# Kernel tuning notes

Measured on AMD Instinct MI355X. Metric: run time of the kernel, lower is better.

Reference implementation:

```python
import jax, jax.numpy as jnp
import numpy as np

BATCH, SEQ_LEN, INPUT_DIM = 64, 8192, 1
RESERVOIR_DIM = 80
DELAY_TAPS = [1, 4, 24, 96, 168]
MAX_DELAY = max(DELAY_TAPS)
SPECTRAL_RADIUS = 0.9
INPUT_SCALING = 0.5
LEAK_RATE = 0.3
SEED = 42
# buf[:, MAX_DELAY - tau] holds h_{t - tau} (zeros if t - tau < 0)
TAP_IDX = np.array([MAX_DELAY - tau for tau in DELAY_TAPS])


def setup_inputs() -> dict:
    key = jax.random.key(0)
    x = jax.random.normal(key, (BATCH, SEQ_LEN, INPUT_DIM), dtype=jnp.float32)
    rng = np.random.default_rng(SEED)
    W_in = rng.uniform(-INPUT_SCALING, INPUT_SCALING, size=(RESERVOIR_DIM, INPUT_DIM))
    W_fb_list = []
    for tau in DELAY_TAPS:
        W_k = rng.standard_normal((RESERVOIR_DIM, RESERVOIR_DIM))
        max_eig = np.max(np.abs(np.linalg.eigvals(W_k)))
        if max_eig > 0:
            W_k = W_k * (SPECTRAL_RADIUS / len(DELAY_TAPS)) / max_eig
        W_fb_list.append(W_k)
    W_fb = np.stack(W_fb_list, axis=0)  # (K, R, R)
    bias = rng.uniform(-0.1, 0.1, size=RESERVOIR_DIM)
    return {
        "x": x,
        "W_in": jnp.asarray(W_in, dtype=jnp.float32),
        "W_fb": jnp.asarray(W_fb, dtype=jnp.float32),
        "bias": jnp.asarray(bias, dtype=jnp.float32),
    }


def reference(x, W_in, W_fb, bias):
    B, S, _ = x.shape
    R = W_in.shape[0]
    # Precompute input drive for all timesteps: (S, B, R) for scan over time.
    drive = jnp.einsum("bsi,ri->sbr", x, W_in)
    h0 = jnp.zeros((B, R), dtype=x.dtype)
    buf0 = jnp.zeros((B, MAX_DELAY, R), dtype=x.dtype)  # rolling history

    def step(carry, drive_t):
        h, buf = carry
        delayed = buf[:, TAP_IDX, :]  # (B, K, R): h_{t-tau} for each tap
        # feedback = sum_k delayed_k @ W_fb_k.T
        feedback = jnp.einsum("bkj,kij->bi", delayed, W_fb)
        h_new = (1.0 - LEAK_RATE) * h + LEAK_RATE * jnp.tanh(drive_t + feedback + bias)
        buf = jnp.concatenate([buf[:, 1:], h_new[:, None, :]], axis=1)
        return (h_new, buf), h_new

    (_, _), states = jax.lax.scan(step, (h0, buf0), drive)
    return jnp.transpose(states, (1, 0, 2))  # (B, S, R)
```

## Files before the change

kernel.cpp:

```cpp
#include <hip/hip_runtime.h>

#define BATCH 64
#define SEQ 8192
#define RDIM 80
#define RING 169
#define NCHUNK (SEQ / 2)

typedef float v2f __attribute__((ext_vector_type(2)));

__device__ __forceinline__ float fast_tanh(float z) {
    float e = __expf(2.0f * z);
    return 1.0f - 2.0f / (e + 1.0f);
}

template <int CTRL>
__device__ __forceinline__ float dpp_xor_add(float v) {
    int o = __builtin_amdgcn_mov_dpp(__float_as_int(v), CTRL, 0xF, 0xF, true);
    return v + __int_as_float(o);
}

__global__ __launch_bounds__(256, 1)
void reservoir_kernel(const float* __restrict__ x,
                      const float* __restrict__ W_in,
                      const float* __restrict__ W_fb,
                      const float* __restrict__ bias,
                      float* __restrict__ out) {
    __shared__ __align__(16) float ring[RING * RDIM];
    __shared__ __align__(16) float h_hist[4 * RDIM];

    const int b    = blockIdx.x;
    const int t    = threadIdx.x;
    const int wid  = t >> 6;
    const int lane = t & 63;

    for (int i = t; i < RING * RDIM; i += 256) ring[i] = 0.0f;
    for (int i = t; i < 4 * RDIM; i += 256) h_hist[i] = 0.0f;

    const float* xb   = x + (size_t)b * SEQ;
    float*       outb = out + (size_t)b * (size_t)SEQ * RDIM;

    v2f wr2[80];

    int q = 0, sub = 0, rowA = 0, rowB = 0;
    float hA = 0.f, hB = 0.f, winA = 0.f, winB = 0.f, bA = 0.f, bB = 0.f;
    v2f hh2[10];
    int tap_tau = 0, qq = 0, half = 0;
    bool tap_valid = false, tap_lo = false;
    float x0 = 0.f, x1 = 0.f;

    if (wid == 0) {
        q = lane >> 2; sub = lane & 3;
        rowA = 5 * q + sub;
        rowB = 5 * q + 4;
        #pragma unroll
        for (int r = 0; r < 5; ++r) {
            const float* src = W_fb + (size_t)(5 * q + r) * RDIM + 20 * sub;
            #pragma unroll
            for (int j4 = 0; j4 < 5; ++j4) {
                float4 v = ((const float4*)src)[j4];
                wr2[r * 10 + 2 * j4 + 0] = (v2f){v.x, v.y};
                wr2[r * 10 + 2 * j4 + 1] = (v2f){v.z, v.w};
            }
        }
        winA = W_in[rowA]; bA = bias[rowA];
        winB = W_in[rowB]; bB = bias[rowB];
        #pragma unroll
        for (int j2 = 0; j2 < 10; ++j2) hh2[j2] = (v2f){0.f, 0.f};
        x0 = xb[0]; x1 = xb[1];
    } else {
        int g = (wid - 1) * 64 + lane;
        tap_valid = (g < 160);
        int gg = tap_valid ? g : 159;
        int k = gg / 40, rem = gg % 40;
        qq = rem >> 1; half = rem & 1;
        tap_lo = (half == 0);
        const int taus[4] = {4, 24, 96, 168};
        tap_tau = taus[k];
        #pragma unroll
        for (int r = 0; r < 4; ++r) {
            const float* src = W_fb + (size_t)(k + 1) * RDIM * RDIM
                                    + (size_t)(4 * qq + r) * RDIM + 40 * half;
            #pragma unroll
            for (int j4 = 0; j4 < 10; ++j4) {
                float4 v = ((const float4*)src)[j4];
                wr2[r * 20 + 2 * j4 + 0] = (v2f){v.x, v.y};
                wr2[r * 20 + 2 * j4 + 1] = (v2f){v.z, v.w};
            }
        }
    }

    __syncthreads();

    for (int c = 0; c < NCHUNK; ++c) {
        if (wid == 0) {
            const int s0  = 2 * c;
            const int sl0 = s0 % RING, sl1 = (s0 + 1) % RING;
            float rgA0 = ring[sl0 * RDIM + rowA];
            float rgA1 = ring[sl1 * RDIM + rowA];
            float rgB0 = 0.f, rgB1 = 0.f;
            if (sub == 0) { rgB0 = ring[sl0 * RDIM + rowB]; rgB1 = ring[sl1 * RDIM + rowB]; }
            ring[sl0 * RDIM + rowA] = 0.f; ring[sl1 * RDIM + rowA] = 0.f;
            if (sub == 0) { ring[sl0 * RDIM + rowB] = 0.f; ring[sl1 * RDIM + rowB] = 0.f; }
            float xn0 = x0, xn1 = x1;
            if (s0 + 2 < SEQ) { float2 xn = *(const float2*)(xb + s0 + 2); xn0 = xn.x; xn1 = xn.y; }

            #pragma unroll
            for (int st = 0; st < 2; ++st) {
                const int s     = s0 + st;
                const float xs  = st ? x1   : x0;
                const float rgA = st ? rgA1 : rgA0;
                const float rgB = st ? rgB1 : rgB0;
                v2f dd2[5];
                #pragma unroll
                for (int r = 0; r < 5; ++r) dd2[r] = (v2f){0.f, 0.f};
                #pragma unroll
                for (int r = 0; r < 5; ++r)
                    #pragma unroll
                    for (int j2 = 0; j2 < 10; ++j2)
                        dd2[r] = __builtin_elementwise_fma(wr2[r * 10 + j2], hh2[j2], dd2[r]);
                float dd[5];
                #pragma unroll
                for (int r = 0; r < 5; ++r) dd[r] = dd2[r].x + dd2[r].y;
                #pragma unroll
                for (int r = 0; r < 5; ++r) {
                    dd[r] = dpp_xor_add<0xB1>(dd[r]);
                    dd[r] = dpp_xor_add<0x4E>(dd[r]);
                }
                float dA = (sub == 0) ? dd[0] : (sub == 1) ? dd[1] : (sub == 2) ? dd[2] : dd[3];
                float zA = dA + rgA + bA + xs * winA;
                hA = 0.7f * hA + 0.3f * fast_tanh(zA);
                if (sub == 0) {
                    float zB = dd[4] + rgB + bB + xs * winB;
                    hB = 0.7f * hB + 0.3f * fast_tanh(zB);
                }
                h_hist[(s & 3) * RDIM + rowA] = hA;
                if (sub == 0) h_hist[(s & 3) * RDIM + rowB] = hB;
                {
                    const float4* hp = (const float4*)(h_hist + (s & 3) * RDIM + 20 * sub);
                    #pragma unroll
                    for (int j4 = 0; j4 < 5; ++j4) {
                        float4 v = hp[j4];
                        hh2[2 * j4 + 0] = (v2f){v.x, v.y};
                        hh2[2 * j4 + 1] = (v2f){v.z, v.w};
                    }
                }
                outb[(size_t)s * RDIM + rowA] = hA;
                if (sub == 0) outb[(size_t)s * RDIM + rowB] = hB;
            }
            x0 = xn0; x1 = xn1;
        } else if (c > 0) {
            const int sp0 = 2 * (c - 1);
            #pragma unroll
            for (int st = 0; st < 2; ++st) {
                const int sp = sp0 + st;
                const float* hp = h_hist + (sp & 3) * RDIM + 40 * half;
                v2f ha2[20];
                #pragma unroll
                for (int j4 = 0; j4 < 10; ++j4) {
                    float4 v = ((const float4*)hp)[j4];
                    ha2[2 * j4 + 0] = (v2f){v.x, v.y};
                    ha2[2 * j4 + 1] = (v2f){v.z, v.w};
                }
                v2f dA2[4];
                #pragma unroll
                for (int r = 0; r < 4; ++r) dA2[r] = (v2f){0.f, 0.f};
                #pragma unroll
                for (int r = 0; r < 4; ++r)
                    #pragma unroll
                    for (int j2 = 0; j2 < 20; ++j2)
                        dA2[r] = __builtin_elementwise_fma(wr2[r * 20 + j2], ha2[j2], dA2[r]);
                float dA[4];
                #pragma unroll
                for (int r = 0; r < 4; ++r) dA[r] = dA2[r].x + dA2[r].y;
                #pragma unroll
                for (int r = 0; r < 4; ++r)
                    dA[r] = dpp_xor_add<0xB1>(dA[r]);
                if (tap_valid && tap_lo) {
                    const int sl = (sp + tap_tau) % RING;
                    float4* pA = (float4*)(ring + sl * RDIM + 4 * qq);
                    float4 vA = *pA;
                    vA.x += dA[0]; vA.y += dA[1]; vA.z += dA[2]; vA.w += dA[3];
                    *pA = vA;
                }
            }
        }
        asm volatile("s_waitcnt lgkmcnt(0)" ::: "memory");
        __builtin_amdgcn_s_barrier();
    }
}

extern "C" void kernel_launch(void* const* d_in, const int* in_sizes, int n_in,
                              void* d_out, int out_size, void* d_ws, size_t ws_size,
                              hipStream_t stream) {
    const float* x    = (const float*)d_in[0];
    const float* W_in = (const float*)d_in[1];
    const float* W_fb = (const float*)d_in[2];
    const float* bias = (const float*)d_in[3];
    float* out        = (float*)d_out;

    reservoir_kernel<<<BATCH, 256, 0, stream>>>(x, W_in, W_fb, bias, out);
}
```

Measured before the change: 3.452 ms.

## Pack two batch elements per 512-thread workgroup

Each workgroup now processes two batch rows with separate ring and history buffers in shared memory, launching half as many blocks with twice the threads. The intent is to share the per-step barrier and improve CU/SIMD utilization. It risks coupling the two recurrences on one barrier and reducing available registers per thread.

```diff
diff --git a/kernel.cpp b/kernel.cpp
--- a/kernel.cpp
+++ b/kernel.cpp
@@ -19,22 +19,27 @@
     return v + __int_as_float(o);
 }
 
-__global__ __launch_bounds__(256, 1)
+__global__ __attribute__((amdgpu_flat_work_group_size(512, 512)))
 void reservoir_kernel(const float* __restrict__ x,
                       const float* __restrict__ W_in,
                       const float* __restrict__ W_fb,
                       const float* __restrict__ bias,
                       float* __restrict__ out) {
-    __shared__ __align__(16) float ring[RING * RDIM];
-    __shared__ __align__(16) float h_hist[4 * RDIM];
-
-    const int b    = blockIdx.x;
+    __shared__ __align__(16) float ring[2 * RING * RDIM];
+    __shared__ __align__(16) float h_hist[2 * 4 * RDIM];
+
     const int t    = threadIdx.x;
     const int wid  = t >> 6;
     const int lane = t & 63;
-
-    for (int i = t; i < RING * RDIM; i += 256) ring[i] = 0.0f;
-    for (int i = t; i < 4 * RDIM; i += 256) h_hist[i] = 0.0f;
+    const int bh   = wid >> 2;
+    const int role = wid & 3;
+    const int b    = blockIdx.x * 2 + bh;
+
+    for (int i = t; i < 2 * RING * RDIM; i += 512) ring[i] = 0.0f;
+    for (int i = t; i < 2 * 4 * RDIM; i += 512) h_hist[i] = 0.0f;
+
+    float* ringp = ring + bh * (RING * RDIM);
+    float* hhp   = h_hist + bh * (4 * RDIM);
 
     const float* xb   = x + (size_t)b * SEQ;
     float*       outb = out + (size_t)b * (size_t)SEQ * RDIM;
@@ -48,7 +53,7 @@
     bool tap_valid = false, tap_lo = false;
     float x0 = 0.f, x1 = 0.f;
 
-    if (wid == 0) {
+    if (role == 0) {
         q = lane >> 2; sub = lane & 3;
         rowA = 5 * q + sub;
         rowB = 5 * q + 4;
@@ -68,7 +73,7 @@
         for (int j2 = 0; j2 < 10; ++j2) hh2[j2] = (v2f){0.f, 0.f};
         x0 = xb[0]; x1 = xb[1];
     } else {
-        int g = (wid - 1) * 64 + lane;
+        int g = (role - 1) * 64 + lane;
         tap_valid = (g < 160);
         int gg = tap_valid ? g : 159;
         int k = gg / 40, rem = gg % 40;
@@ -92,15 +97,15 @@
     __syncthreads();
 
     for (int c = 0; c < NCHUNK; ++c) {
-        if (wid == 0) {
+        if (role == 0) {
             const int s0  = 2 * c;
             const int sl0 = s0 % RING, sl1 = (s0 + 1) % RING;
-            float rgA0 = ring[sl0 * RDIM + rowA];
-            float rgA1 = ring[sl1 * RDIM + rowA];
+            float rgA0 = ringp[sl0 * RDIM + rowA];
+            float rgA1 = ringp[sl1 * RDIM + rowA];
             float rgB0 = 0.f, rgB1 = 0.f;
-            if (sub == 0) { rgB0 = ring[sl0 * RDIM + rowB]; rgB1 = ring[sl1 * RDIM + rowB]; }
-            ring[sl0 * RDIM + rowA] = 0.f; ring[sl1 * RDIM + rowA] = 0.f;
-            if (sub == 0) { ring[sl0 * RDIM + rowB] = 0.f; ring[sl1 * RDIM + rowB] = 0.f; }
+            if (sub == 0) { rgB0 = ringp[sl0 * RDIM + rowB]; rgB1 = ringp[sl1 * RDIM + rowB]; }
+            ringp[sl0 * RDIM + rowA] = 0.f; ringp[sl1 * RDIM + rowA] = 0.f;
+            if (sub == 0) { ringp[sl0 * RDIM + rowB] = 0.f; ringp[sl1 * RDIM + rowB] = 0.f; }
             float xn0 = x0, xn1 = x1;
             if (s0 + 2 < SEQ) { float2 xn = *(const float2*)(xb + s0 + 2); xn0 = xn.x; xn1 = xn.y; }
 
@@ -133,10 +138,10 @@
                     float zB = dd[4] + rgB + bB + xs * winB;
                     hB = 0.7f * hB + 0.3f * fast_tanh(zB);
                 }
-                h_hist[(s & 3) * RDIM + rowA] = hA;
-                if (sub == 0) h_hist[(s & 3) * RDIM + rowB] = hB;
+                hhp[(s & 3) * RDIM + rowA] = hA;
+                if (sub == 0) hhp[(s & 3) * RDIM + rowB] = hB;
                 {
-                    const float4* hp = (const float4*)(h_hist + (s & 3) * RDIM + 20 * sub);
+                    const float4* hp = (const float4*)(hhp + (s & 3) * RDIM + 20 * sub);
                     #pragma unroll
                     for (int j4 = 0; j4 < 5; ++j4) {
                         float4 v = hp[j4];
@@ -153,7 +158,7 @@
             #pragma unroll
             for (int st = 0; st < 2; ++st) {
                 const int sp = sp0 + st;
-                const float* hp = h_hist + (sp & 3) * RDIM + 40 * half;
+                const float* hp = hhp + (sp & 3) * RDIM + 40 * half;
                 v2f ha2[20];
                 #pragma unroll
                 for (int j4 = 0; j4 < 10; ++j4) {
@@ -177,7 +182,7 @@
                     dA[r] = dpp_xor_add<0xB1>(dA[r]);
                 if (tap_valid && tap_lo) {
                     const int sl = (sp + tap_tau) % RING;
-                    float4* pA = (float4*)(ring + sl * RDIM + 4 * qq);
+                    float4* pA = (float4*)(ringp + sl * RDIM + 4 * qq);
                     float4 vA = *pA;
                     vA.x += dA[0]; vA.y += dA[1]; vA.z += dA[2]; vA.w += dA[3];
                     *pA = vA;
@@ -198,5 +203,5 @@
     const float* bias = (const float*)d_in[3];
     float* out        = (float*)d_out;
 
-    reservoir_kernel<<<BATCH, 256, 0, stream>>>(x, W_in, W_fb, bias, out);
-}
+    reservoir_kernel<<<BATCH / 2, 512, 0, stream>>>(x, W_in, W_fb, bias, out);
+}
```

After: 4.863 ms. +40.9%, slower.
